# Kernel tuning notes

Measured on AMD Instinct MI355X. Metric: run time of the kernel, lower is better.

## Reference

```python
import jax, jax.numpy as jnp
import numpy as np

B, T, FEA = 8, 4096, 512      # input: fea = 2*IN_C real values
IN_C = FEA // 2               # complex input units
H_C = 256                     # complex hidden units (hidden_size init arg)
NUM_LAYERS = 2


def _clin(x, wr, wi, br, bi):
    """Complex linear: x=[..., 2*in] (real half then imag half) -> [..., 2*out]."""
    xr, xi = jnp.split(x, 2, axis=-1)
    yr = xr @ wr - xi @ wi + br
    yi = xr @ wi + xi @ wr + bi
    return jnp.concatenate([yr, yi], axis=-1)


def _rnn_layer(x, wr, wi, wbr, wbi, ur, ui, ubr, ubi):
    # x: [B, T, 2*in_c] -> h: [B, T, 2*H_C]
    wx = _clin(x, wr, wi, wbr, wbi)          # [B, T, 2*H_C] (input proj, one big GEMM)
    wx_t = jnp.swapaxes(wx, 0, 1)            # [T, B, 2*H_C] for scan over time
    h0 = jnp.zeros((x.shape[0], 2 * H_C), dtype=x.dtype)  # h_init = zeros

    def step(h, wt):
        h_new = jnp.tanh(wt + _clin(h, ur, ui, ubr, ubi))  # act(w_t + U h); eval drop_mask=1
        return h_new, h_new

    _, hs = jax.lax.scan(step, h0, wx_t)     # [T, B, 2*H_C]
    return jnp.swapaxes(hs, 0, 1)            # [B, T, 2*H_C]


def setup_inputs() -> dict:
    key = jax.random.key(0)
    ks = jax.random.split(key, 1 + 8 * NUM_LAYERS)
    inp = {"x": jax.random.normal(ks[0], (B, T, FEA), dtype=jnp.float32)}
    in_c = IN_C
    ki = 1
    for l in range(NUM_LAYERS):
        sw = 1.0 / np.sqrt(2.0 * in_c)   # glorot-ish scale for input proj
        su = 1.0 / np.sqrt(2.0 * H_C)    # recurrent weight scale (keeps tanh unsaturated)
        inp[f"l{l}_wr"] = jax.random.normal(ks[ki + 0], (in_c, H_C), jnp.float32) * sw
        inp[f"l{l}_wi"] = jax.random.normal(ks[ki + 1], (in_c, H_C), jnp.float32) * sw
        inp[f"l{l}_wbr"] = jnp.zeros((H_C,), jnp.float32)
        inp[f"l{l}_wbi"] = jnp.zeros((H_C,), jnp.float32)
        inp[f"l{l}_ur"] = jax.random.normal(ks[ki + 2], (H_C, H_C), jnp.float32) * su
        inp[f"l{l}_ui"] = jax.random.normal(ks[ki + 3], (H_C, H_C), jnp.float32) * su
        inp[f"l{l}_ubr"] = jnp.zeros((H_C,), jnp.float32)
        inp[f"l{l}_ubi"] = jnp.zeros((H_C,), jnp.float32)
        ki += 4
        in_c = H_C  # next layer consumes 2*H_C real values -> H_C complex
    return inp


def reference(x,
              l0_wr, l0_wi, l0_wbr, l0_wbi, l0_ur, l0_ui, l0_ubr, l0_ubi,
              l1_wr, l1_wi, l1_wbr, l1_wbi, l1_ur, l1_ui, l1_ubr, l1_ubi):
    h = _rnn_layer(x, l0_wr, l0_wi, l0_wbr, l0_wbi, l0_ur, l0_ui, l0_ubr, l0_ubi)
    h = _rnn_layer(h, l1_wr, l1_wi, l1_wbr, l1_wbi, l1_ur, l1_ui, l1_ubr, l1_ubi)
    return h  # [B, T, 2*H_C]
```

## Files before the change

### kernel.cpp

```cpp
#include <hip/hip_runtime.h>

typedef unsigned int uint;
typedef unsigned long long u64;
typedef __attribute__((ext_vector_type(4))) float f32x4;
typedef __attribute__((ext_vector_type(8))) short s16x8;

union U4 { uint u[4]; s16x8 v; uint4 q; };

#define TT 4096
#define HC2 512
#define SENT 0xFFFFFFFFu

__device__ __forceinline__ uint bf16_rne(float f) {
  uint x = __float_as_uint(f);
  x += 0x7fffu + ((x >> 16) & 1u);
  return x >> 16;
}
__device__ __forceinline__ uint pack_split(float f) {
  uint hi = bf16_rne(f);
  float fh = __uint_as_float(hi << 16);
  uint lo = bf16_rne(f - fh);
  return hi | (lo << 16);
}
__device__ __forceinline__ float fast_tanh(float y) {
  float e = __builtin_amdgcn_exp2f(y * 2.885390081777927f);
  return 1.0f - 2.0f * __builtin_amdgcn_rcpf(e + 1.0f);
}

__device__ __forceinline__ void st_sys(uint* p, uint v) {
  asm volatile("global_store_dword %0, %1, off sc0 sc1" :: "v"(p), "v"(v) : "memory");
}
__device__ __forceinline__ uint ld1_sys(const uint* p) {
  uint w;
  asm volatile("global_load_dword %0, %1, off sc0 sc1\n\t"
               "s_waitcnt vmcnt(0)" : "=&v"(w) : "v"(p) : "memory");
  return w;
}
__device__ __forceinline__ void ld16_sys(const uint* p, uint4& a, uint4& b, uint4& c, uint4& d) {
  asm volatile("global_load_dwordx4 %0, %4, off sc0 sc1\n\t"
               "global_load_dwordx4 %1, %4, off offset:16 sc0 sc1\n\t"
               "global_load_dwordx4 %2, %4, off offset:32 sc0 sc1\n\t"
               "global_load_dwordx4 %3, %4, off offset:48 sc0 sc1\n\t"
               "s_waitcnt vmcnt(0)"
               : "=&v"(a), "=&v"(b), "=&v"(c), "=&v"(d) : "v"(p) : "memory");
}
__device__ __forceinline__ void ld32_sys(const uint* pa, const uint* pb,
                                         uint4& a, uint4& b, uint4& c, uint4& d,
                                         uint4& e, uint4& f, uint4& g, uint4& h) {
  asm volatile("global_load_dwordx4 %0, %8, off sc0 sc1\n\t"
               "global_load_dwordx4 %1, %8, off offset:16 sc0 sc1\n\t"
               "global_load_dwordx4 %2, %8, off offset:32 sc0 sc1\n\t"
               "global_load_dwordx4 %3, %8, off offset:48 sc0 sc1\n\t"
               "global_load_dwordx4 %4, %9, off sc0 sc1\n\t"
               "global_load_dwordx4 %5, %9, off offset:16 sc0 sc1\n\t"
               "global_load_dwordx4 %6, %9, off offset:32 sc0 sc1\n\t"
               "global_load_dwordx4 %7, %9, off offset:48 sc0 sc1\n\t"
               "s_waitcnt vmcnt(0)"
               : "=&v"(a), "=&v"(b), "=&v"(c), "=&v"(d),
                 "=&v"(e), "=&v"(f), "=&v"(g), "=&v"(h)
               : "v"(pa), "v"(pb) : "memory");
}

__global__ void pack_weights_kernel(const float* __restrict__ wr, const float* __restrict__ wi,
                                    const float* __restrict__ wbr, const float* __restrict__ wbi,
                                    const float* __restrict__ ur, const float* __restrict__ ui,
                                    const float* __restrict__ ubr, const float* __restrict__ ubi,
                                    uint* __restrict__ MwT, uint* __restrict__ MuT,
                                    float* __restrict__ bias) {
  const int id = blockIdx.x * 256 + threadIdx.x;
  const int j = id >> 9, k = id & 511;
  const int jj = j & 255, kk = k & 255;
  float mw, mu;
  if (k < 256) {
    if (j < 256) { mw =  wr[kk * 256 + jj]; mu =  ur[kk * 256 + jj]; }
    else         { mw =  wi[kk * 256 + jj]; mu =  ui[kk * 256 + jj]; }
  } else {
    if (j < 256) { mw = -wi[kk * 256 + jj]; mu = -ui[kk * 256 + jj]; }
    else         { mw =  wr[kk * 256 + jj]; mu =  ur[kk * 256 + jj]; }
  }
  MwT[id] = pack_split(mw);
  MuT[id] = pack_split(mu);
  if (id < 512)
    bias[id] = (id < 256) ? (wbr[id] + ubr[id]) : (wbi[id - 256] + ubi[id - 256]);
}

__global__ void pack_x_kernel(const float* __restrict__ x, uint* __restrict__ xp) {
  const u64 i = ((u64)blockIdx.x * 256 + threadIdx.x) * 4;
  float4 v = *(const float4*)(x + i);
  uint4 o;
  o.x = pack_split(v.x); o.y = pack_split(v.y);
  o.z = pack_split(v.z); o.w = pack_split(v.w);
  *(uint4*)(xp + i) = o;
}

__global__ __launch_bounds__(256, 2)
void gemm_split_kernel(const uint* __restrict__ A, const uint* __restrict__ BT,
                       const float* __restrict__ bias, float* __restrict__ C) {
  __shared__ __align__(16) uint a_s[128][36];
  __shared__ __align__(16) uint b_s[128][36];
  const int tid = threadIdx.x;
  const int wv = tid >> 6, lane = tid & 63;
  const int q = lane >> 4, cl = lane & 15;
  const int row0 = (int)blockIdx.x * 128, col0 = (int)blockIdx.y * 128;
  const int wro = (wv >> 1) * 64, wco = (wv & 1) * 64;
  const int sr = tid >> 1, sc = (tid & 1) * 16;

  f32x4 acc[4][4];
#pragma unroll
  for (int a = 0; a < 4; ++a)
#pragma unroll
    for (int b = 0; b < 4; ++b) acc[a][b] = (f32x4){0.f, 0.f, 0.f, 0.f};

  const uint* ga = A + (u64)(row0 + sr) * 512 + sc;
  const uint* gb = BT + (u64)(col0 + sr) * 512 + sc;

  for (int kb = 0; kb < 16; ++kb) {
    uint4 va0 = *(const uint4*)(ga + 0), va1 = *(const uint4*)(ga + 4);
    uint4 va2 = *(const uint4*)(ga + 8), va3 = *(const uint4*)(ga + 12);
    uint4 vb0 = *(const uint4*)(gb + 0), vb1 = *(const uint4*)(gb + 4);
    uint4 vb2 = *(const uint4*)(gb + 8), vb3 = *(const uint4*)(gb + 12);
    ga += 32; gb += 32;
    __syncthreads();
    *(uint4*)&a_s[sr][sc + 0] = va0;  *(uint4*)&a_s[sr][sc + 4] = va1;
    *(uint4*)&a_s[sr][sc + 8] = va2;  *(uint4*)&a_s[sr][sc + 12] = va3;
    *(uint4*)&b_s[sr][sc + 0] = vb0;  *(uint4*)&b_s[sr][sc + 4] = vb1;
    *(uint4*)&b_s[sr][sc + 8] = vb2;  *(uint4*)&b_s[sr][sc + 12] = vb3;
    __syncthreads();

    s16x8 ah[4], al[4];
#pragma unroll
    for (int rt = 0; rt < 4; ++rt) {
      const uint* p = &a_s[wro + rt * 16 + cl][q * 8];
      uint4 p0 = *(const uint4*)(p), p1 = *(const uint4*)(p + 4);
      U4 th, tl;
      th.u[0] = (p0.x & 0xffffu) | (p0.y << 16);
      th.u[1] = (p0.z & 0xffffu) | (p0.w << 16);
      th.u[2] = (p1.x & 0xffffu) | (p1.y << 16);
      th.u[3] = (p1.z & 0xffffu) | (p1.w << 16);
      tl.u[0] = (p0.x >> 16) | (p0.y & 0xffff0000u);
      tl.u[1] = (p0.z >> 16) | (p0.w & 0xffff0000u);
      tl.u[2] = (p1.x >> 16) | (p1.y & 0xffff0000u);
      tl.u[3] = (p1.z >> 16) | (p1.w & 0xffff0000u);
      ah[rt] = th.v; al[rt] = tl.v;
    }
#pragma unroll
    for (int ct = 0; ct < 4; ++ct) {
      const uint* p = &b_s[wco + ct * 16 + cl][q * 8];
      uint4 p0 = *(const uint4*)(p), p1 = *(const uint4*)(p + 4);
      U4 th, tl;
      th.u[0] = (p0.x & 0xffffu) | (p0.y << 16);
      th.u[1] = (p0.z & 0xffffu) | (p0.w << 16);
      th.u[2] = (p1.x & 0xffffu) | (p1.y << 16);
      th.u[3] = (p1.z & 0xffffu) | (p1.w << 16);
      tl.u[0] = (p0.x >> 16) | (p0.y & 0xffff0000u);
      tl.u[1] = (p0.z >> 16) | (p0.w & 0xffff0000u);
      tl.u[2] = (p1.x >> 16) | (p1.y & 0xffff0000u);
      tl.u[3] = (p1.z >> 16) | (p1.w & 0xffff0000u);
#pragma unroll
      for (int rt = 0; rt < 4; ++rt) {
        acc[rt][ct] = __builtin_amdgcn_mfma_f32_16x16x32_bf16(ah[rt], th.v, acc[rt][ct], 0, 0, 0);
        acc[rt][ct] = __builtin_amdgcn_mfma_f32_16x16x32_bf16(al[rt], th.v, acc[rt][ct], 0, 0, 0);
        acc[rt][ct] = __builtin_amdgcn_mfma_f32_16x16x32_bf16(ah[rt], tl.v, acc[rt][ct], 0, 0, 0);
      }
    }
  }
#pragma unroll
  for (int ct = 0; ct < 4; ++ct) {
    const int col = col0 + wco + ct * 16 + cl;
    const float bv = bias[col];
#pragma unroll
    for (int rt = 0; rt < 4; ++rt) {
      const int rbase = row0 + wro + rt * 16 + q * 4;
#pragma unroll
      for (int r2 = 0; r2 < 4; ++r2)
        C[(u64)(rbase + r2) * 512 + col] = acc[rt][ct][r2] + bv;
    }
  }
}

__global__ __launch_bounds__(256, 1)
void fused_scan_kernel(const uint* __restrict__ MuT0, const float* __restrict__ wxb,
                       const uint* __restrict__ MwT1, const uint* __restrict__ MuT1,
                       const float* __restrict__ bias1,
                       uint* __restrict__ xpk0,
                       uint* __restrict__ h1x) {
  __shared__ __align__(16) unsigned short xah[16][520];
  __shared__ __align__(16) unsigned short xal[16][520];
  __shared__ __align__(16) unsigned short yah[16][520];
  __shared__ __align__(16) unsigned short yal[16][520];
  const int tid = threadIdx.x;
  const int wv = tid >> 6, lane = tid & 63;
  const int q = lane >> 4, cl = lane & 15;
  const int layer = (int)blockIdx.x >> 3;
  const int blk = (int)blockIdx.x & 7;
  const int j = blk * 64 + wv * 16 + cl;

  for (int idx = tid; idx < 16 * 520; idx += 256) {
    ((unsigned short*)xah)[idx] = 0; ((unsigned short*)xal)[idx] = 0;
    ((unsigned short*)yah)[idx] = 0; ((unsigned short*)yal)[idx] = 0;
  }

  uint4 bh4[16], bl4[16];
  {
    const uint* urow = (layer ? MuT1 : MuT0) + (u64)j * 512;
#pragma unroll
    for (int ks = 0; ks < 16; ++ks) {
      const int k0 = ks * 32 + q * 8;
      uint4 p0 = *(const uint4*)(urow + k0);
      uint4 p1 = *(const uint4*)(urow + k0 + 4);
      uint4 h, l;
      h.x = (p0.x & 0xffffu) | (p0.y << 16);
      h.y = (p0.z & 0xffffu) | (p0.w << 16);
      h.z = (p1.x & 0xffffu) | (p1.y << 16);
      h.w = (p1.z & 0xffffu) | (p1.w << 16);
      l.x = (p0.x >> 16) | (p0.y & 0xffff0000u);
      l.y = (p0.z >> 16) | (p0.w & 0xffff0000u);
      l.z = (p1.x >> 16) | (p1.y & 0xffff0000u);
      l.w = (p1.z >> 16) | (p1.w & 0xffff0000u);
      bh4[ks] = h; bl4[ks] = l;
    }
  }
  uint4 ch4[16], cl4[16];
  if (layer) {
    const uint* wrow = MwT1 + (u64)j * 512;
#pragma unroll
    for (int ks = 0; ks < 16; ++ks) {
      const int k0 = ks * 32 + q * 8;
      uint4 p0 = *(const uint4*)(wrow + k0);
      uint4 p1 = *(const uint4*)(wrow + k0 + 4);
      uint4 h, l;
      h.x = (p0.x & 0xffffu) | (p0.y << 16);
      h.y = (p0.z & 0xffffu) | (p0.w << 16);
      h.z = (p1.x & 0xffffu) | (p1.y << 16);
      h.w = (p1.z & 0xffffu) | (p1.w << 16);
      l.x = (p0.x >> 16) | (p0.y & 0xffff0000u);
      l.y = (p0.z >> 16) | (p0.w & 0xffff0000u);
      l.z = (p1.x >> 16) | (p1.y & 0xffff0000u);
      l.w = (p1.z >> 16) | (p1.w & 0xffff0000u);
      ch4[ks] = h; cl4[ks] = l;
    }
  }
  __syncthreads();

  const int srow = tid >> 5;
  const int scol = (tid & 31) * 16;
  bool timeout = false;

  if (layer == 0) {
    const uint* hsrc_base = xpk0 + (u64)srow * TT * HC2 + scol;
#pragma unroll 1
    for (int t = 0; t < TT; ++t) {
      float wpre[4] = {0.f, 0.f, 0.f, 0.f};
      if (q < 2) {
#pragma unroll
        for (int r = 0; r < 4; ++r)
          wpre[r] = wxb[((u64)(q * 4 + r) * TT + t) * HC2 + j];
      }

      f32x4 acc0 = {0.f, 0.f, 0.f, 0.f}, acc1 = acc0, acc2 = acc0;
      if (t > 0) {
        const uint* src = hsrc_base + (u64)(t - 1) * HC2;
        uint4 p0, p1, p2, p3;
        int spin = 0;
        for (;;) {
          uint w = ld1_sys(src);
          if (__ballot(timeout || w != SENT) == ~0ull) break;
          if (++spin > (1 << 20)) { timeout = true; break; }
          __builtin_amdgcn_s_sleep(1);
        }
        spin = 0;
        for (;;) {
          ld16_sys(src, p0, p1, p2, p3);
          bool ok = timeout ||
                    (p0.x != SENT && p0.y != SENT && p0.z != SENT && p0.w != SENT &&
                     p1.x != SENT && p1.y != SENT && p1.z != SENT && p1.w != SENT &&
                     p2.x != SENT && p2.y != SENT && p2.z != SENT && p2.w != SENT &&
                     p3.x != SENT && p3.y != SENT && p3.z != SENT && p3.w != SENT);
          if (__ballot(ok) == ~0ull) break;
          if (++spin > (1 << 20)) { timeout = true; break; }
        }
        {
          uint pcs[16] = {p0.x, p0.y, p0.z, p0.w, p1.x, p1.y, p1.z, p1.w,
                          p2.x, p2.y, p2.z, p2.w, p3.x, p3.y, p3.z, p3.w};
          U4 h0, h1, l0, l1;
#pragma unroll
          for (int e = 0; e < 4; ++e) {
            h0.u[e] = (pcs[2 * e] & 0xffffu) | (pcs[2 * e + 1] << 16);
            l0.u[e] = (pcs[2 * e] >> 16) | (pcs[2 * e + 1] & 0xffff0000u);
            h1.u[e] = (pcs[8 + 2 * e] & 0xffffu) | (pcs[8 + 2 * e + 1] << 16);
            l1.u[e] = (pcs[8 + 2 * e] >> 16) | (pcs[8 + 2 * e + 1] & 0xffff0000u);
          }
          *(uint4*)&xah[srow][scol] = h0.q;  *(uint4*)&xah[srow][scol + 8] = h1.q;
          *(uint4*)&xal[srow][scol] = l0.q;  *(uint4*)&xal[srow][scol + 8] = l1.q;
        }
        __syncthreads();
#pragma unroll
        for (int ks = 0; ks < 16; ++ks) {
          const int k0 = ks * 32 + q * 8;
          s16x8 ah = *(const s16x8*)&xah[cl][k0];
          s16x8 al = *(const s16x8*)&xal[cl][k0];
          U4 tb, tc;
          tb.q = bh4[ks];
          tc.q = bl4[ks];
          acc0 = __builtin_amdgcn_mfma_f32_16x16x32_bf16(ah, tb.v, acc0, 0, 0, 0);
          acc1 = __builtin_amdgcn_mfma_f32_16x16x32_bf16(al, tb.v, acc1, 0, 0, 0);
          acc2 = __builtin_amdgcn_mfma_f32_16x16x32_bf16(ah, tc.v, acc2, 0, 0, 0);
        }
      }
      if (q < 2) {
#pragma unroll
        for (int r = 0; r < 4; ++r) {
          const int b = q * 4 + r;
          const u64 off = ((u64)b * TT + t) * HC2 + j;
          float y = acc0[r] + acc1[r] + acc2[r] + wpre[r];
          float h = fast_tanh(y);
          st_sys(xpk0 + off, pack_split(h));
        }
      }
    }
  } else {
    const uint* h0src_base = xpk0 + (u64)srow * TT * HC2 + scol;
    const uint* h1src_base = h1x + (u64)srow * TT * HC2 + scol;
    const float bv = bias1[j];
#pragma unroll 1
    for (int t = 0; t < TT; ++t) {
      const uint* s0p = h0src_base + (u64)t * HC2;
      uint4 q0, q1, q2, q3, p0, p1, p2, p3;
      int spin = 0;
      if (t == 0) {
        p0 = make_uint4(0u, 0u, 0u, 0u); p1 = p0; p2 = p0; p3 = p0;
        for (;;) {
          uint w = ld1_sys(s0p);
          if (__ballot(timeout || w != SENT) == ~0ull) break;
          if (++spin > (1 << 20)) { timeout = true; break; }
          __builtin_amdgcn_s_sleep(1);
        }
        spin = 0;
        for (;;) {
          ld16_sys(s0p, q0, q1, q2, q3);
          bool ok = timeout ||
                    (q0.x != SENT && q0.y != SENT && q0.z != SENT && q0.w != SENT &&
                     q1.x != SENT && q1.y != SENT && q1.z != SENT && q1.w != SENT &&
                     q2.x != SENT && q2.y != SENT && q2.z != SENT && q2.w != SENT &&
                     q3.x != SENT && q3.y != SENT && q3.z != SENT && q3.w != SENT);
          if (__ballot(ok) == ~0ull) break;
          if (++spin > (1 << 20)) { timeout = true; break; }
        }
      } else {
        const uint* s1p = h1src_base + (u64)(t - 1) * HC2;
        for (;;) {
          uint w0 = ld1_sys(s0p);
          uint w1 = ld1_sys(s1p);
          if (__ballot(timeout || (w0 != SENT && w1 != SENT)) == ~0ull) break;
          if (++spin > (1 << 20)) { timeout = true; break; }
          __builtin_amdgcn_s_sleep(1);
        }
        spin = 0;
        for (;;) {
          ld32_sys(s0p, s1p, q0, q1, q2, q3, p0, p1, p2, p3);
          bool ok = timeout ||
                    (q0.x != SENT && q0.y != SENT && q0.z != SENT && q0.w != SENT &&
                     q1.x != SENT && q1.y != SENT && q1.z != SENT && q1.w != SENT &&
                     q2.x != SENT && q2.y != SENT && q2.z != SENT && q2.w != SENT &&
                     q3.x != SENT && q3.y != SENT && q3.z != SENT && q3.w != SENT &&
                     p0.x != SENT && p0.y != SENT && p0.z != SENT && p0.w != SENT &&
                     p1.x != SENT && p1.y != SENT && p1.z != SENT && p1.w != SENT &&
                     p2.x != SENT && p2.y != SENT && p2.z != SENT && p2.w != SENT &&
                     p3.x != SENT && p3.y != SENT && p3.z != SENT && p3.w != SENT);
          if (__ballot(ok) == ~0ull) break;
          if (++spin > (1 << 20)) { timeout = true; break; }
        }
      }
      {
        uint pcs[16] = {q0.x, q0.y, q0.z, q0.w, q1.x, q1.y, q1.z, q1.w,
                        q2.x, q2.y, q2.z, q2.w, q3.x, q3.y, q3.z, q3.w};
        U4 h0, h1, l0, l1;
#pragma unroll
        for (int e = 0; e < 4; ++e) {
          h0.u[e] = (pcs[2 * e] & 0xffffu) | (pcs[2 * e + 1] << 16);
          l0.u[e] = (pcs[2 * e] >> 16) | (pcs[2 * e + 1] & 0xffff0000u);
          h1.u[e] = (pcs[8 + 2 * e] & 0xffffu) | (pcs[8 + 2 * e + 1] << 16);
          l1.u[e] = (pcs[8 + 2 * e] >> 16) | (pcs[8 + 2 * e + 1] & 0xffff0000u);
        }
        *(uint4*)&yah[srow][scol] = h0.q;  *(uint4*)&yah[srow][scol + 8] = h1.q;
        *(uint4*)&yal[srow][scol] = l0.q;  *(uint4*)&yal[srow][scol + 8] = l1.q;
      }
      {
        uint pf[16] = {p0.x, p0.y, p0.z, p0.w, p1.x, p1.y, p1.z, p1.w,
                       p2.x, p2.y, p2.z, p2.w, p3.x, p3.y, p3.z, p3.w};
        U4 H0, H1, L0, L1;
#pragma unroll
        for (int e = 0; e < 4; ++e) {
          float fa = __uint_as_float(pf[2 * e]);
          float fb = __uint_as_float(pf[2 * e + 1]);
          uint ha = bf16_rne(fa), hb = bf16_rne(fb);
          uint la = bf16_rne(fa - __uint_as_float(ha << 16));
          uint lb = bf16_rne(fb - __uint_as_float(hb << 16));
          H0.u[e] = ha | (hb << 16);
          L0.u[e] = la | (lb << 16);
          float fc = __uint_as_float(pf[8 + 2 * e]);
          float fd = __uint_as_float(pf[8 + 2 * e + 1]);
          uint hc = bf16_rne(fc), hd = bf16_rne(fd);
          uint lc = bf16_rne(fc - __uint_as_float(hc << 16));
          uint ld = bf16_rne(fd - __uint_as_float(hd << 16));
          H1.u[e] = hc | (hd << 16);
          L1.u[e] = lc | (ld << 16);
        }
        *(uint4*)&xah[srow][scol] = H0.q;  *(uint4*)&xah[srow][scol + 8] = H1.q;
        *(uint4*)&xal[srow][scol] = L0.q;  *(uint4*)&xal[srow][scol + 8] = L1.q;
      }
      __syncthreads();

      f32x4 aU0 = {0.f, 0.f, 0.f, 0.f}, aU1 = aU0, aU2 = aU0;
      f32x4 aW0 = aU0, aW1 = aU0, aW2 = aU0;
#pragma unroll
      for (int ks = 0; ks < 16; ++ks) {
        const int k0 = ks * 32 + q * 8;
        s16x8 ah = *(const s16x8*)&xah[cl][k0];
        s16x8 al = *(const s16x8*)&xal[cl][k0];
        s16x8 yh = *(const s16x8*)&yah[cl][k0];
        s16x8 yl = *(const s16x8*)&yal[cl][k0];
        U4 tb, tc, td, te;
        tb.q = bh4[ks]; tc.q = bl4[ks];
        td.q = ch4[ks]; te.q = cl4[ks];
        aU0 = __builtin_amdgcn_mfma_f32_16x16x32_bf16(ah, tb.v, aU0, 0, 0, 0);
        aW0 = __builtin_amdgcn_mfma_f32_16x16x32_bf16(yh, td.v, aW0, 0, 0, 0);
        aU1 = __builtin_amdgcn_mfma_f32_16x16x32_bf16(al, tb.v, aU1, 0, 0, 0);
        aW1 = __builtin_amdgcn_mfma_f32_16x16x32_bf16(yl, td.v, aW1, 0, 0, 0);
        aU2 = __builtin_amdgcn_mfma_f32_16x16x32_bf16(ah, tc.v, aU2, 0, 0, 0);
        aW2 = __builtin_amdgcn_mfma_f32_16x16x32_bf16(yh, te.v, aW2, 0, 0, 0);
      }
      if (q < 2) {
#pragma unroll
        for (int r = 0; r < 4; ++r) {
          const int b = q * 4 + r;
          const u64 off = ((u64)b * TT + t) * HC2 + j;
          float y = aU0[r] + aU1[r] + aU2[r] + aW0[r] + aW1[r] + aW2[r] + bv;
          float h = fast_tanh(y);
          st_sys(h1x + off, __float_as_uint(h));
        }
      }
    }
  }
}

extern "C" void kernel_launch(void* const* d_in, const int* in_sizes, int n_in,
                              void* d_out, int out_size, void* d_ws, size_t ws_size,
                              hipStream_t stream) {
  const float* x = (const float*)d_in[0];
  const float* L0[8]; const float* L1[8];
  for (int i = 0; i < 8; ++i) { L0[i] = (const float*)d_in[1 + i]; L1[i] = (const float*)d_in[9 + i]; }

  char* ws = (char*)d_ws;
  const size_t MB = 1024 * 1024;
  uint* MwT0 = (uint*)(ws + 0 * MB);
  uint* MuT0 = (uint*)(ws + 1 * MB);
  uint* MwT1 = (uint*)(ws + 2 * MB);
  uint* MuT1 = (uint*)(ws + 3 * MB);
  float* bias0 = (float*)(ws + 4 * MB);
  float* bias1 = (float*)(ws + 4 * MB + 8192);
  uint* Apk = (uint*)(ws + 8 * MB);
  float* wx = (float*)(ws + 72 * MB);

  pack_weights_kernel<<<1024, 256, 0, stream>>>(L0[0], L0[1], L0[2], L0[3], L0[4], L0[5], L0[6], L0[7],
                                                MwT0, MuT0, bias0);
  pack_weights_kernel<<<1024, 256, 0, stream>>>(L1[0], L1[1], L1[2], L1[3], L1[4], L1[5], L1[6], L1[7],
                                                MwT1, MuT1, bias1);
  pack_x_kernel<<<16384, 256, 0, stream>>>(x, Apk);
  gemm_split_kernel<<<dim3(256, 4), 256, 0, stream>>>(Apk, MwT0, bias0, wx);
  hipMemsetAsync(Apk, 0xFF, 64 * MB, stream);
  hipMemsetAsync(d_out, 0xFF, 64 * MB, stream);
  fused_scan_kernel<<<16, 256, 0, stream>>>(MuT0, wx, MwT1, MuT1, bias1, Apk, (uint*)d_out);
}
```

Measured before the change: 14.22 ms.

## Replace sentinel-word polling with per-timestep atomic counter flags

Each wave now drains its stores with a waitcnt and atomically bumps a per-timestep counter, and consumers spin on that counter until all 32 waves of the producing layer have arrived. Previously consumers spun on a single sentinel word in the data itself. The coarse first poll now waits for the whole step instead of one word, while the full sentinel-checking reload loop stays in place. This adds an atomic per wave per step and a flag memset, and it relies on the waitcnt acting as a sufficient release for system-scope stores.

```diff
diff --git a/kernel.cpp b/kernel.cpp
--- a/kernel.cpp
+++ b/kernel.cpp
@@ -10,6 +10,7 @@
 #define TT 4096
 #define HC2 512
 #define SENT 0xFFFFFFFFu
+#define WAVES_PER_LAYER 32u
 
 __device__ __forceinline__ uint bf16_rne(float f) {
   uint x = __float_as_uint(f);
@@ -59,6 +60,9 @@
                : "=&v"(a), "=&v"(b), "=&v"(c), "=&v"(d),
                  "=&v"(e), "=&v"(f), "=&v"(g), "=&v"(h)
                : "v"(pa), "v"(pb) : "memory");
+}
+__device__ __forceinline__ void release_fence() {
+  asm volatile("s_waitcnt vmcnt(0)" ::: "memory");
 }
 
 __global__ void pack_weights_kernel(const float* __restrict__ wr, const float* __restrict__ wi,
@@ -183,7 +187,9 @@
                        const uint* __restrict__ MwT1, const uint* __restrict__ MuT1,
                        const float* __restrict__ bias1,
                        uint* __restrict__ xpk0,
-                       uint* __restrict__ h1x) {
+                       uint* __restrict__ h1x,
+                       uint* __restrict__ flag0,
+                       uint* __restrict__ flag1) {
   __shared__ __align__(16) unsigned short xah[16][520];
   __shared__ __align__(16) unsigned short xal[16][520];
   __shared__ __align__(16) unsigned short yah[16][520];
@@ -262,9 +268,10 @@
         const uint* src = hsrc_base + (u64)(t - 1) * HC2;
         uint4 p0, p1, p2, p3;
         int spin = 0;
-        for (;;) {
-          uint w = ld1_sys(src);
-          if (__ballot(timeout || w != SENT) == ~0ull) break;
+        const uint* fp = flag0 + (t - 1);
+        for (;;) {
+          uint fv = ld1_sys(fp);
+          if (__ballot(timeout || fv >= WAVES_PER_LAYER) == ~0ull) break;
           if (++spin > (1 << 20)) { timeout = true; break; }
           __builtin_amdgcn_s_sleep(1);
         }
@@ -317,6 +324,8 @@
           st_sys(xpk0 + off, pack_split(h));
         }
       }
+      release_fence();
+      if (lane == 0) atomicAdd(flag0 + t, 1u);
     }
   } else {
     const uint* h0src_base = xpk0 + (u64)srow * TT * HC2 + scol;
@@ -329,9 +338,10 @@
       int spin = 0;
       if (t == 0) {
         p0 = make_uint4(0u, 0u, 0u, 0u); p1 = p0; p2 = p0; p3 = p0;
-        for (;;) {
-          uint w = ld1_sys(s0p);
-          if (__ballot(timeout || w != SENT) == ~0ull) break;
+        const uint* fp = flag0 + t;
+        for (;;) {
+          uint fv = ld1_sys(fp);
+          if (__ballot(timeout || fv >= WAVES_PER_LAYER) == ~0ull) break;
           if (++spin > (1 << 20)) { timeout = true; break; }
           __builtin_amdgcn_s_sleep(1);
         }
@@ -348,10 +358,12 @@
         }
       } else {
         const uint* s1p = h1src_base + (u64)(t - 1) * HC2;
-        for (;;) {
-          uint w0 = ld1_sys(s0p);
-          uint w1 = ld1_sys(s1p);
-          if (__ballot(timeout || (w0 != SENT && w1 != SENT)) == ~0ull) break;
+        const uint* fp0 = flag0 + t;
+        const uint* fp1 = flag1 + (t - 1);
+        for (;;) {
+          uint f0v = ld1_sys(fp0);
+          uint f1v = ld1_sys(fp1);
+          if (__ballot(timeout || (f0v >= WAVES_PER_LAYER && f1v >= WAVES_PER_LAYER)) == ~0ull) break;
           if (++spin > (1 << 20)) { timeout = true; break; }
           __builtin_amdgcn_s_sleep(1);
         }
@@ -440,6 +452,8 @@
           st_sys(h1x + off, __float_as_uint(h));
         }
       }
+      release_fence();
+      if (lane == 0) atomicAdd(flag1 + t, 1u);
     }
   }
 }
@@ -459,6 +473,8 @@
   uint* MuT1 = (uint*)(ws + 3 * MB);
   float* bias0 = (float*)(ws + 4 * MB);
   float* bias1 = (float*)(ws + 4 * MB + 8192);
+  uint* flag0 = (uint*)(ws + 5 * MB);
+  uint* flag1 = (uint*)(ws + 5 * MB + TT * 4);
   uint* Apk = (uint*)(ws + 8 * MB);
   float* wx = (float*)(ws + 72 * MB);
 
@@ -470,5 +486,7 @@
   gemm_split_kernel<<<dim3(256, 4), 256, 0, stream>>>(Apk, MwT0, bias0, wx);
   hipMemsetAsync(Apk, 0xFF, 64 * MB, stream);
   hipMemsetAsync(d_out, 0xFF, 64 * MB, stream);
-  fused_scan_kernel<<<16, 256, 0, stream>>>(MuT0, wx, MwT1, MuT1, bias1, Apk, (uint*)d_out);
-}
+  hipMemsetAsync(flag0, 0, 2 * TT * 4, stream);
+  fused_scan_kernel<<<16, 256, 0, stream>>>(MuT0, wx, MwT1, MuT1, bias1, Apk, (uint*)d_out,
+                                            flag0, flag1);
+}
```

New measurement: 18.96 ms. 33.4% more time.

## Split layer-1 input projection into separate block role to shorten recurrent critical path

Applied to the files above, without the earlier changes.

Adds a third block role, 8 more blocks, that computes the layer-1 input projection W·h0_t plus bias and publishes it as split-bf16 words in a new flag-polled buffer. The layer-1 recurrent blocks then do only the U·h1 MFMAs per step and poll both that buffer and their own previous hidden state. This takes half the per-step MFMA work and the LDS staging for layer 0's output off the serial layer-1 chain. In exchange it adds another 64MB sentinel memset, extra global traffic and another cross-block dependency whose polling latency may offset the savings.

```diff
diff --git a/kernel.cpp b/kernel.cpp
--- a/kernel.cpp
+++ b/kernel.cpp
@@ -21,6 +21,9 @@
   float fh = __uint_as_float(hi << 16);
   uint lo = bf16_rne(f - fh);
   return hi | (lo << 16);
+}
+__device__ __forceinline__ float unpack_split(uint w) {
+  return __uint_as_float(w << 16) + __uint_as_float(w & 0xffff0000u);
 }
 __device__ __forceinline__ float fast_tanh(float y) {
   float e = __builtin_amdgcn_exp2f(y * 2.885390081777927f);
@@ -44,21 +47,35 @@
                "s_waitcnt vmcnt(0)"
                : "=&v"(a), "=&v"(b), "=&v"(c), "=&v"(d) : "v"(p) : "memory");
 }
-__device__ __forceinline__ void ld32_sys(const uint* pa, const uint* pb,
-                                         uint4& a, uint4& b, uint4& c, uint4& d,
-                                         uint4& e, uint4& f, uint4& g, uint4& h) {
+__device__ __forceinline__ void ld16z_sys(const uint* p, const uint* zp,
+                                          uint4& a, uint4& b, uint4& c, uint4& d,
+                                          uint& z0, uint& z1, uint& z2, uint& z3) {
   asm volatile("global_load_dwordx4 %0, %8, off sc0 sc1\n\t"
                "global_load_dwordx4 %1, %8, off offset:16 sc0 sc1\n\t"
                "global_load_dwordx4 %2, %8, off offset:32 sc0 sc1\n\t"
                "global_load_dwordx4 %3, %8, off offset:48 sc0 sc1\n\t"
-               "global_load_dwordx4 %4, %9, off sc0 sc1\n\t"
-               "global_load_dwordx4 %5, %9, off offset:16 sc0 sc1\n\t"
-               "global_load_dwordx4 %6, %9, off offset:32 sc0 sc1\n\t"
-               "global_load_dwordx4 %7, %9, off offset:48 sc0 sc1\n\t"
+               "global_load_dword %4, %9, off sc0 sc1\n\t"
+               "global_load_dword %5, %9, off offset:256 sc0 sc1\n\t"
+               "global_load_dword %6, %9, off offset:512 sc0 sc1\n\t"
+               "global_load_dword %7, %9, off offset:768 sc0 sc1\n\t"
                "s_waitcnt vmcnt(0)"
                : "=&v"(a), "=&v"(b), "=&v"(c), "=&v"(d),
-                 "=&v"(e), "=&v"(f), "=&v"(g), "=&v"(h)
-               : "v"(pa), "v"(pb) : "memory");
+                 "=&v"(z0), "=&v"(z1), "=&v"(z2), "=&v"(z3)
+               : "v"(p), "v"(zp) : "memory");
+}
+__device__ __forceinline__ void ld2_sys(const uint* pa, const uint* pb, uint& a, uint& b) {
+  asm volatile("global_load_dword %0, %2, off sc0 sc1\n\t"
+               "global_load_dword %1, %3, off sc0 sc1\n\t"
+               "s_waitcnt vmcnt(0)"
+               : "=&v"(a), "=&v"(b) : "v"(pa), "v"(pb) : "memory");
+}
+__device__ __forceinline__ void ld4z_sys(const uint* zp, uint& z0, uint& z1, uint& z2, uint& z3) {
+  asm volatile("global_load_dword %0, %4, off sc0 sc1\n\t"
+               "global_load_dword %1, %4, off offset:256 sc0 sc1\n\t"
+               "global_load_dword %2, %4, off offset:512 sc0 sc1\n\t"
+               "global_load_dword %3, %4, off offset:768 sc0 sc1\n\t"
+               "s_waitcnt vmcnt(0)"
+               : "=&v"(z0), "=&v"(z1), "=&v"(z2), "=&v"(z3) : "v"(zp) : "memory");
 }
 
 __global__ void pack_weights_kernel(const float* __restrict__ wr, const float* __restrict__ wi,
@@ -183,46 +200,26 @@
                        const uint* __restrict__ MwT1, const uint* __restrict__ MuT1,
                        const float* __restrict__ bias1,
                        uint* __restrict__ xpk0,
-                       uint* __restrict__ h1x) {
+                       uint* __restrict__ h1x,
+                       uint* __restrict__ zbuf) {
   __shared__ __align__(16) unsigned short xah[16][520];
   __shared__ __align__(16) unsigned short xal[16][520];
-  __shared__ __align__(16) unsigned short yah[16][520];
-  __shared__ __align__(16) unsigned short yal[16][520];
   const int tid = threadIdx.x;
   const int wv = tid >> 6, lane = tid & 63;
   const int q = lane >> 4, cl = lane & 15;
-  const int layer = (int)blockIdx.x >> 3;
+  const int role = (int)blockIdx.x >> 3;
   const int blk = (int)blockIdx.x & 7;
   const int j = blk * 64 + wv * 16 + cl;
+  const int jc = wv * 16 + cl;
 
   for (int idx = tid; idx < 16 * 520; idx += 256) {
     ((unsigned short*)xah)[idx] = 0; ((unsigned short*)xal)[idx] = 0;
-    ((unsigned short*)yah)[idx] = 0; ((unsigned short*)yal)[idx] = 0;
   }
 
   uint4 bh4[16], bl4[16];
   {
-    const uint* urow = (layer ? MuT1 : MuT0) + (u64)j * 512;
-#pragma unroll
-    for (int ks = 0; ks < 16; ++ks) {
-      const int k0 = ks * 32 + q * 8;
-      uint4 p0 = *(const uint4*)(urow + k0);
-      uint4 p1 = *(const uint4*)(urow + k0 + 4);
-      uint4 h, l;
-      h.x = (p0.x & 0xffffu) | (p0.y << 16);
-      h.y = (p0.z & 0xffffu) | (p0.w << 16);
-      h.z = (p1.x & 0xffffu) | (p1.y << 16);
-      h.w = (p1.z & 0xffffu) | (p1.w << 16);
-      l.x = (p0.x >> 16) | (p0.y & 0xffff0000u);
-      l.y = (p0.z >> 16) | (p0.w & 0xffff0000u);
-      l.z = (p1.x >> 16) | (p1.y & 0xffff0000u);
-      l.w = (p1.z >> 16) | (p1.w & 0xffff0000u);
-      bh4[ks] = h; bl4[ks] = l;
-    }
-  }
-  uint4 ch4[16], cl4[16];
-  if (layer) {
-    const uint* wrow = MwT1 + (u64)j * 512;
+    const uint* wsel = (role == 0) ? MuT0 : ((role == 1) ? MwT1 : MuT1);
+    const uint* wrow = wsel + (u64)j * 512;
 #pragma unroll
     for (int ks = 0; ks < 16; ++ks) {
       const int k0 = ks * 32 + q * 8;
@@ -237,7 +234,7 @@
       l.y = (p0.z >> 16) | (p0.w & 0xffff0000u);
       l.z = (p1.x >> 16) | (p1.y & 0xffff0000u);
       l.w = (p1.z >> 16) | (p1.w & 0xffff0000u);
-      ch4[ks] = h; cl4[ks] = l;
+      bh4[ks] = h; bl4[ks] = l;
     }
   }
   __syncthreads();
@@ -246,7 +243,7 @@
   const int scol = (tid & 31) * 16;
   bool timeout = false;
 
-  if (layer == 0) {
+  if (role == 0) {
     const uint* hsrc_base = xpk0 + (u64)srow * TT * HC2 + scol;
 #pragma unroll 1
     for (int t = 0; t < TT; ++t) {
@@ -256,7 +253,6 @@
         for (int r = 0; r < 4; ++r)
           wpre[r] = wxb[((u64)(q * 4 + r) * TT + t) * HC2 + j];
       }
-
       f32x4 acc0 = {0.f, 0.f, 0.f, 0.f}, acc1 = acc0, acc2 = acc0;
       if (t > 0) {
         const uint* src = hsrc_base + (u64)(t - 1) * HC2;
@@ -299,9 +295,7 @@
           const int k0 = ks * 32 + q * 8;
           s16x8 ah = *(const s16x8*)&xah[cl][k0];
           s16x8 al = *(const s16x8*)&xal[cl][k0];
-          U4 tb, tc;
-          tb.q = bh4[ks];
-          tc.q = bl4[ks];
+          U4 tb, tc; tb.q = bh4[ks]; tc.q = bl4[ks];
           acc0 = __builtin_amdgcn_mfma_f32_16x16x32_bf16(ah, tb.v, acc0, 0, 0, 0);
           acc1 = __builtin_amdgcn_mfma_f32_16x16x32_bf16(al, tb.v, acc1, 0, 0, 0);
           acc2 = __builtin_amdgcn_mfma_f32_16x16x32_bf16(ah, tc.v, acc2, 0, 0, 0);
@@ -313,67 +307,38 @@
           const int b = q * 4 + r;
           const u64 off = ((u64)b * TT + t) * HC2 + j;
           float y = acc0[r] + acc1[r] + acc2[r] + wpre[r];
-          float h = fast_tanh(y);
-          st_sys(xpk0 + off, pack_split(h));
-        }
-      }
-    }
-  } else {
+          st_sys(xpk0 + off, pack_split(fast_tanh(y)));
+        }
+      }
+    }
+  } else if (role == 1) {
     const uint* h0src_base = xpk0 + (u64)srow * TT * HC2 + scol;
-    const uint* h1src_base = h1x + (u64)srow * TT * HC2 + scol;
     const float bv = bias1[j];
 #pragma unroll 1
     for (int t = 0; t < TT; ++t) {
-      const uint* s0p = h0src_base + (u64)t * HC2;
-      uint4 q0, q1, q2, q3, p0, p1, p2, p3;
+      const uint* src = h0src_base + (u64)t * HC2;
+      uint4 p0, p1, p2, p3;
       int spin = 0;
-      if (t == 0) {
-        p0 = make_uint4(0u, 0u, 0u, 0u); p1 = p0; p2 = p0; p3 = p0;
-        for (;;) {
-          uint w = ld1_sys(s0p);
-          if (__ballot(timeout || w != SENT) == ~0ull) break;
-          if (++spin > (1 << 20)) { timeout = true; break; }
-          __builtin_amdgcn_s_sleep(1);
-        }
-        spin = 0;
-        for (;;) {
-          ld16_sys(s0p, q0, q1, q2, q3);
-          bool ok = timeout ||
-                    (q0.x != SENT && q0.y != SENT && q0.z != SENT && q0.w != SENT &&
-                     q1.x != SENT && q1.y != SENT && q1.z != SENT && q1.w != SENT &&
-                     q2.x != SENT && q2.y != SENT && q2.z != SENT && q2.w != SENT &&
-                     q3.x != SENT && q3.y != SENT && q3.z != SENT && q3.w != SENT);
-          if (__ballot(ok) == ~0ull) break;
-          if (++spin > (1 << 20)) { timeout = true; break; }
-        }
-      } else {
-        const uint* s1p = h1src_base + (u64)(t - 1) * HC2;
-        for (;;) {
-          uint w0 = ld1_sys(s0p);
-          uint w1 = ld1_sys(s1p);
-          if (__ballot(timeout || (w0 != SENT && w1 != SENT)) == ~0ull) break;
-          if (++spin > (1 << 20)) { timeout = true; break; }
-          __builtin_amdgcn_s_sleep(1);
-        }
-        spin = 0;
-        for (;;) {
-          ld32_sys(s0p, s1p, q0, q1, q2, q3, p0, p1, p2, p3);
-          bool ok = timeout ||
-                    (q0.x != SENT && q0.y != SENT && q0.z != SENT && q0.w != SENT &&
-                     q1.x != SENT && q1.y != SENT && q1.z != SENT && q1.w != SENT &&
-                     q2.x != SENT && q2.y != SENT && q2.z != SENT && q2.w != SENT &&
-                     q3.x != SENT && q3.y != SENT && q3.z != SENT && q3.w != SENT &&
-                     p0.x != SENT && p0.y != SENT && p0.z != SENT && p0.w != SENT &&
-                     p1.x != SENT && p1.y != SENT && p1.z != SENT && p1.w != SENT &&
-                     p2.x != SENT && p2.y != SENT && p2.z != SENT && p2.w != SENT &&
-                     p3.x != SENT && p3.y != SENT && p3.z != SENT && p3.w != SENT);
-          if (__ballot(ok) == ~0ull) break;
-          if (++spin > (1 << 20)) { timeout = true; break; }
-        }
+      for (;;) {
+        uint w = ld1_sys(src);
+        if (__ballot(timeout || w != SENT) == ~0ull) break;
+        if (++spin > (1 << 20)) { timeout = true; break; }
+        __builtin_amdgcn_s_sleep(1);
+      }
+      spin = 0;
+      for (;;) {
+        ld16_sys(src, p0, p1, p2, p3);
+        bool ok = timeout ||
+                  (p0.x != SENT && p0.y != SENT && p0.z != SENT && p0.w != SENT &&
+                   p1.x != SENT && p1.y != SENT && p1.z != SENT && p1.w != SENT &&
+                   p2.x != SENT && p2.y != SENT && p2.z != SENT && p2.w != SENT &&
+                   p3.x != SENT && p3.y != SENT && p3.z != SENT && p3.w != SENT);
+        if (__ballot(ok) == ~0ull) break;
+        if (++spin > (1 << 20)) { timeout = true; break; }
       }
       {
-        uint pcs[16] = {q0.x, q0.y, q0.z, q0.w, q1.x, q1.y, q1.z, q1.w,
-                        q2.x, q2.y, q2.z, q2.w, q3.x, q3.y, q3.z, q3.w};
+        uint pcs[16] = {p0.x, p0.y, p0.z, p0.w, p1.x, p1.y, p1.z, p1.w,
+                        p2.x, p2.y, p2.z, p2.w, p3.x, p3.y, p3.z, p3.w};
         U4 h0, h1, l0, l1;
 #pragma unroll
         for (int e = 0; e < 4; ++e) {
@@ -382,62 +347,125 @@
           h1.u[e] = (pcs[8 + 2 * e] & 0xffffu) | (pcs[8 + 2 * e + 1] << 16);
           l1.u[e] = (pcs[8 + 2 * e] >> 16) | (pcs[8 + 2 * e + 1] & 0xffff0000u);
         }
-        *(uint4*)&yah[srow][scol] = h0.q;  *(uint4*)&yah[srow][scol + 8] = h1.q;
-        *(uint4*)&yal[srow][scol] = l0.q;  *(uint4*)&yal[srow][scol + 8] = l1.q;
-      }
-      {
-        uint pf[16] = {p0.x, p0.y, p0.z, p0.w, p1.x, p1.y, p1.z, p1.w,
-                       p2.x, p2.y, p2.z, p2.w, p3.x, p3.y, p3.z, p3.w};
-        U4 H0, H1, L0, L1;
-#pragma unroll
-        for (int e = 0; e < 4; ++e) {
-          float fa = __uint_as_float(pf[2 * e]);
-          float fb = __uint_as_float(pf[2 * e + 1]);
-          uint ha = bf16_rne(fa), hb = bf16_rne(fb);
-          uint la = bf16_rne(fa - __uint_as_float(ha << 16));
-          uint lb = bf16_rne(fb - __uint_as_float(hb << 16));
-          H0.u[e] = ha | (hb << 16);
-          L0.u[e] = la | (lb << 16);
-          float fc = __uint_as_float(pf[8 + 2 * e]);
-          float fd = __uint_as_float(pf[8 + 2 * e + 1]);
-          uint hc = bf16_rne(fc), hd = bf16_rne(fd);
-          uint lc = bf16_rne(fc - __uint_as_float(hc << 16));
-          uint ld = bf16_rne(fd - __uint_as_float(hd << 16));
-          H1.u[e] = hc | (hd << 16);
-          L1.u[e] = lc | (ld << 16);
-        }
-        *(uint4*)&xah[srow][scol] = H0.q;  *(uint4*)&xah[srow][scol + 8] = H1.q;
-        *(uint4*)&xal[srow][scol] = L0.q;  *(uint4*)&xal[srow][scol + 8] = L1.q;
+        *(uint4*)&xah[srow][scol] = h0.q;  *(uint4*)&xah[srow][scol + 8] = h1.q;
+        *(uint4*)&xal[srow][scol] = l0.q;  *(uint4*)&xal[srow][scol + 8] = l1.q;
       }
       __syncthreads();
-
-      f32x4 aU0 = {0.f, 0.f, 0.f, 0.f}, aU1 = aU0, aU2 = aU0;
-      f32x4 aW0 = aU0, aW1 = aU0, aW2 = aU0;
+      f32x4 a0 = {0.f, 0.f, 0.f, 0.f}, a1 = a0, a2 = a0;
 #pragma unroll
       for (int ks = 0; ks < 16; ++ks) {
         const int k0 = ks * 32 + q * 8;
-        s16x8 ah = *(const s16x8*)&xah[cl][k0];
-        s16x8 al = *(const s16x8*)&xal[cl][k0];
-        s16x8 yh = *(const s16x8*)&yah[cl][k0];
-        s16x8 yl = *(const s16x8*)&yal[cl][k0];
-        U4 tb, tc, td, te;
-        tb.q = bh4[ks]; tc.q = bl4[ks];
-        td.q = ch4[ks]; te.q = cl4[ks];
-        aU0 = __builtin_amdgcn_mfma_f32_16x16x32_bf16(ah, tb.v, aU0, 0, 0, 0);
-        aW0 = __builtin_amdgcn_mfma_f32_16x16x32_bf16(yh, td.v, aW0, 0, 0, 0);
-        aU1 = __builtin_amdgcn_mfma_f32_16x16x32_bf16(al, tb.v, aU1, 0, 0, 0);
-        aW1 = __builtin_amdgcn_mfma_f32_16x16x32_bf16(yl, td.v, aW1, 0, 0, 0);
-        aU2 = __builtin_amdgcn_mfma_f32_16x16x32_bf16(ah, tc.v, aU2, 0, 0, 0);
-        aW2 = __builtin_amdgcn_mfma_f32_16x16x32_bf16(yh, te.v, aW2, 0, 0, 0);
+        s16x8 yh = *(const s16x8*)&xah[cl][k0];
+        s16x8 yl = *(const s16x8*)&xal[cl][k0];
+        U4 tb, tc; tb.q = bh4[ks]; tc.q = bl4[ks];
+        a0 = __builtin_amdgcn_mfma_f32_16x16x32_bf16(yh, tb.v, a0, 0, 0, 0);
+        a1 = __builtin_amdgcn_mfma_f32_16x16x32_bf16(yl, tb.v, a1, 0, 0, 0);
+        a2 = __builtin_amdgcn_mfma_f32_16x16x32_bf16(yh, tc.v, a2, 0, 0, 0);
       }
       if (q < 2) {
+        uint* zo = zbuf + (((u64)blk * TT + t) * 8 + q * 4) * 64 + jc;
+#pragma unroll
+        for (int r = 0; r < 4; ++r) {
+          float z = a0[r] + a1[r] + a2[r] + bv;
+          st_sys(zo + r * 64, pack_split(z));
+        }
+      }
+      __syncthreads();
+    }
+  } else {
+    const uint* h1src_base = h1x + (u64)srow * TT * HC2 + scol;
+#pragma unroll 1
+    for (int t = 0; t < TT; ++t) {
+      const uint* zp = zbuf + ((q < 2) ? ((((u64)blk * TT + t) * 8 + q * 4) * 64 + jc) : 0);
+      uint zw0, zw1, zw2, zw3;
+      int spin = 0;
+      if (t == 0) {
+        for (;;) {
+          uint z0 = ld1_sys(zp);
+          if (__ballot(timeout || q >= 2 || z0 != SENT) == ~0ull) break;
+          if (++spin > (1 << 20)) { timeout = true; break; }
+          __builtin_amdgcn_s_sleep(1);
+        }
+        spin = 0;
+        for (;;) {
+          ld4z_sys(zp, zw0, zw1, zw2, zw3);
+          bool ok = timeout || q >= 2 ||
+                    (zw0 != SENT && zw1 != SENT && zw2 != SENT && zw3 != SENT);
+          if (__ballot(ok) == ~0ull) break;
+          if (++spin > (1 << 20)) { timeout = true; break; }
+        }
+        __syncthreads();
+      } else {
+        const uint* src = h1src_base + (u64)(t - 1) * HC2;
+        uint4 p0, p1, p2, p3;
+        for (;;) {
+          uint w0, z0;
+          ld2_sys(src, zp, w0, z0);
+          bool ok = timeout || (w0 != SENT && (q >= 2 || z0 != SENT));
+          if (__ballot(ok) == ~0ull) break;
+          if (++spin > (1 << 20)) { timeout = true; break; }
+          __builtin_amdgcn_s_sleep(1);
+        }
+        spin = 0;
+        for (;;) {
+          ld16z_sys(src, zp, p0, p1, p2, p3, zw0, zw1, zw2, zw3);
+          bool ok = timeout ||
+                    ((p0.x != SENT && p0.y != SENT && p0.z != SENT && p0.w != SENT &&
+                      p1.x != SENT && p1.y != SENT && p1.z != SENT && p1.w != SENT &&
+                      p2.x != SENT && p2.y != SENT && p2.z != SENT && p2.w != SENT &&
+                      p3.x != SENT && p3.y != SENT && p3.z != SENT && p3.w != SENT) &&
+                     (q >= 2 ||
+                      (zw0 != SENT && zw1 != SENT && zw2 != SENT && zw3 != SENT)));
+          if (__ballot(ok) == ~0ull) break;
+          if (++spin > (1 << 20)) { timeout = true; break; }
+        }
+        {
+          uint pf[16] = {p0.x, p0.y, p0.z, p0.w, p1.x, p1.y, p1.z, p1.w,
+                         p2.x, p2.y, p2.z, p2.w, p3.x, p3.y, p3.z, p3.w};
+          U4 H0, H1, L0, L1;
+#pragma unroll
+          for (int e = 0; e < 4; ++e) {
+            float fa = __uint_as_float(pf[2 * e]);
+            float fb = __uint_as_float(pf[2 * e + 1]);
+            uint ha = bf16_rne(fa), hb = bf16_rne(fb);
+            uint la = bf16_rne(fa - __uint_as_float(ha << 16));
+            uint lb = bf16_rne(fb - __uint_as_float(hb << 16));
+            H0.u[e] = ha | (hb << 16);
+            L0.u[e] = la | (lb << 16);
+            float fc = __uint_as_float(pf[8 + 2 * e]);
+            float fd = __uint_as_float(pf[8 + 2 * e + 1]);
+            uint hc = bf16_rne(fc), hd = bf16_rne(fd);
+            uint lc = bf16_rne(fc - __uint_as_float(hc << 16));
+            uint ld = bf16_rne(fd - __uint_as_float(hd << 16));
+            H1.u[e] = hc | (hd << 16);
+            L1.u[e] = lc | (ld << 16);
+          }
+          *(uint4*)&xah[srow][scol] = H0.q;  *(uint4*)&xah[srow][scol + 8] = H1.q;
+          *(uint4*)&xal[srow][scol] = L0.q;  *(uint4*)&xal[srow][scol + 8] = L1.q;
+        }
+        __syncthreads();
+      }
+      f32x4 a0 = {0.f, 0.f, 0.f, 0.f}, a1 = a0, a2 = a0;
+      if (t > 0) {
+#pragma unroll
+        for (int ks = 0; ks < 16; ++ks) {
+          const int k0 = ks * 32 + q * 8;
+          s16x8 ah = *(const s16x8*)&xah[cl][k0];
+          s16x8 al = *(const s16x8*)&xal[cl][k0];
+          U4 tb, tc; tb.q = bh4[ks]; tc.q = bl4[ks];
+          a0 = __builtin_amdgcn_mfma_f32_16x16x32_bf16(ah, tb.v, a0, 0, 0, 0);
+          a1 = __builtin_amdgcn_mfma_f32_16x16x32_bf16(al, tb.v, a1, 0, 0, 0);
+          a2 = __builtin_amdgcn_mfma_f32_16x16x32_bf16(ah, tc.v, a2, 0, 0, 0);
+        }
+      }
+      if (q < 2) {
+        uint zw[4] = {zw0, zw1, zw2, zw3};
 #pragma unroll
         for (int r = 0; r < 4; ++r) {
           const int b = q * 4 + r;
           const u64 off = ((u64)b * TT + t) * HC2 + j;
-          float y = aU0[r] + aU1[r] + aU2[r] + aW0[r] + aW1[r] + aW2[r] + bv;
-          float h = fast_tanh(y);
-          st_sys(h1x + off, __float_as_uint(h));
+          float y = a0[r] + a1[r] + a2[r] + unpack_split(zw[r]);
+          st_sys(h1x + off, __float_as_uint(fast_tanh(y)));
         }
       }
     }
@@ -461,6 +489,7 @@
   float* bias1 = (float*)(ws + 4 * MB + 8192);
   uint* Apk = (uint*)(ws + 8 * MB);
   float* wx = (float*)(ws + 72 * MB);
+  uint* zbuf = (uint*)(ws + 136 * MB);
 
   pack_weights_kernel<<<1024, 256, 0, stream>>>(L0[0], L0[1], L0[2], L0[3], L0[4], L0[5], L0[6], L0[7],
                                                 MwT0, MuT0, bias0);
@@ -470,5 +499,6 @@
   gemm_split_kernel<<<dim3(256, 4), 256, 0, stream>>>(Apk, MwT0, bias0, wx);
   hipMemsetAsync(Apk, 0xFF, 64 * MB, stream);
   hipMemsetAsync(d_out, 0xFF, 64 * MB, stream);
-  fused_scan_kernel<<<16, 256, 0, stream>>>(MuT0, wx, MwT1, MuT1, bias1, Apk, (uint*)d_out);
-}
+  hipMemsetAsync(zbuf, 0xFF, 64 * MB, stream);
+  fused_scan_kernel<<<24, 256, 0, stream>>>(MuT0, wx, MwT1, MuT1, bias1, Apk, (uint*)d_out, zbuf);
+}
```

Result: faster. 12.20 ms (-14.2%).
